# Optimization experiments

Hardware: AMD Instinct MI355X
Metric: run time of the kernel (lower is better)

The kernel has to match this reference:

```python
import jax, jax.numpy as jnp
import numpy as np

NUM_HEADS = 12
KSIZE = 3
PAD = 1


def setup_inputs() -> dict:
    key = jax.random.key(0)
    ks = jax.random.split(key, 5)
    B, H, W, C = 4, 96, 96, 192
    x = jax.random.normal(ks[0], (B, H * W, C), jnp.float32)
    Wq = jax.random.normal(ks[1], (W, W), jnp.float32) * 0.02
    bq = jnp.zeros((W,), jnp.float32)
    Wkv = jax.random.normal(ks[2], (2 * W, W), jnp.float32) * 0.02
    bkv = jnp.zeros((2 * W,), jnp.float32)
    Wp = jax.random.normal(ks[3], (C, C), jnp.float32) * 0.02
    bp = jnp.zeros((C,), jnp.float32)
    f_qr = jnp.float32(1.0)
    f_kr = jnp.float32(1.0)
    f_vr = jnp.float32(1.0)
    return {"x": x, "Wq": Wq, "bq": bq, "Wkv": Wkv, "bkv": bkv, "Wp": Wp,
            "bp": bp, "f_qr": f_qr, "f_kr": f_kr, "f_vr": f_vr, "H": H, "W": W}


def reference(x, Wq, bq, Wkv, bkv, Wp, bp, f_qr, f_kr, f_vr, H, W):
    B, N, C = x.shape
    nh = NUM_HEADS
    hc = C // nh
    scale = C ** (-0.5)
    # faithful to torch: raw reshape of (B, N, C) into (B, C, H, W)
    xn = x.reshape(B, C, H, W)
    # q_proj is Linear over the last (width) axis, size Hw == W
    q = jnp.einsum('bchw,vw->bchv', xn, Wq) + bq            # (B,C,H,W)
    q = q.reshape(B, H, W, nh, hc).transpose(0, 3, 1, 2, 4)  # (B,nh,H,W,hc)
    q = (q * scale * f_qr).reshape(B, nh, H * W, hc)         # (B,nh,L,hc)
    # kv_proj: Linear(W -> 2W) over last axis
    kv = jnp.einsum('bchw,vw->bchv', xn, Wkv) + bkv          # (B,C,H,2W)
    kv = kv.reshape(B, H, W, 2, nh, hc).transpose(3, 0, 4, 5, 1, 2)  # (2,B,nh,hc,H,W)
    kv = jnp.pad(kv, ((0, 0),) * 4 + ((PAD, PAD), (PAD, PAD)))       # zero-pad spatial
    # unfold: 3x3 sliding windows, stride 1 -> one window per pixel
    patches = jnp.stack([kv[..., i:i + H, j:j + W]
                         for i in range(KSIZE) for j in range(KSIZE)], axis=4)
    # (2,B,nh,hc,9,H,W) -> (2,B,nh,L,9,hc); kernel index = kh*3+kw matches nn.Unfold
    patches = patches.reshape(2, B, nh, hc, KSIZE * KSIZE, H * W).transpose(0, 1, 2, 5, 4, 3)
    k = patches[0] * f_kr                                    # (B,nh,L,9,hc)
    v = patches[1] * f_vr
    attn = jax.nn.softmax(jnp.einsum('bnlc,bnlkc->bnlk', q, k), axis=-1)  # (B,nh,L,9)
    out = jnp.einsum('bnlk,bnlkc->bnlc', attn, v)            # (B,nh,L,hc)
    out = out.transpose(0, 2, 1, 3).reshape(B, H, W, C)      # (B,H,W,C)
    out = jnp.einsum('bhwc,oc->bhwo', out, Wp) + bp          # proj Linear(dim,dim)
    return out.reshape(B, H * W, C)
```

## Files before the change

### kernel.cpp

```cpp
#include <hip/hip_runtime.h>

#define HW2   96
#define NH    12
#define LPIX  (HW2*HW2)
#define BATCH 4

typedef __attribute__((ext_vector_type(8))) short bf16x8;
typedef __attribute__((ext_vector_type(4))) float f32x4;

static __device__ __forceinline__ float bf2f(unsigned short u) {
  union { unsigned int i; float f; } v; v.i = ((unsigned int)u) << 16; return v.f;
}
static __device__ __forceinline__ unsigned short f2bf(float f) {
  union { float f; unsigned int i; } v; v.f = f;
  unsigned int r = v.i + 0x7FFF + ((v.i >> 16) & 1);
  return (unsigned short)(r >> 16);
}

__global__ __launch_bounds__(256) void cvt_w_kernel(
    const float* __restrict__ Wq, const float* __restrict__ Wkv,
    const float* __restrict__ Wp,
    unsigned short* __restrict__ wqb, unsigned short* __restrict__ wkvb,
    unsigned short* __restrict__ wpb) {
  int i = blockIdx.x * 256 + threadIdx.x;
  if (i < 9216)       wqb[i]          = f2bf(Wq[i]);
  else if (i < 27648) wkvb[i - 9216]  = f2bf(Wkv[i - 9216]);
  else if (i < 64512) wpb[i - 27648]  = f2bf(Wp[i - 27648]);
}

__global__ __launch_bounds__(256, 4) void qkv_gemm(
    const float* __restrict__ X,
    const unsigned short* __restrict__ wq, const unsigned short* __restrict__ wkv,
    const float* __restrict__ bq, const float* __restrict__ bkv,
    const float* __restrict__ fqr, const float* __restrict__ fkr,
    const float* __restrict__ fvr,
    unsigned short* __restrict__ Qb, unsigned short* __restrict__ KVb)
{
  const int tid  = threadIdx.x;
  const int r0   = blockIdx.x * 64;
  const int lane = tid & 63, w = tid >> 6;
  const int col  = lane & 15;
  const int koff = (lane >> 4) * 8;
  const int arow = r0 + 16 * w + (lane & 15);
  const int rbase = r0 + 16 * w + 4 * (lane >> 4);

  const float* xr = X + (size_t)arow * 96;
  float xv[24];
  *(float4*)&xv[0]  = *(const float4*)(xr + koff);
  *(float4*)&xv[4]  = *(const float4*)(xr + koff + 4);
  *(float4*)&xv[8]  = *(const float4*)(xr + koff + 32);
  *(float4*)&xv[12] = *(const float4*)(xr + koff + 36);
  *(float4*)&xv[16] = *(const float4*)(xr + koff + 64);
  *(float4*)&xv[20] = *(const float4*)(xr + koff + 68);
  unsigned short au[24];
  #pragma unroll
  for (int j = 0; j < 24; j++) au[j] = f2bf(xv[j]);
  bf16x8 af0 = *(const bf16x8*)&au[0];
  bf16x8 af1 = *(const bf16x8*)&au[8];
  bf16x8 af2 = *(const bf16x8*)&au[16];

  const float fqr0 = fqr[0] * 0.07216878364870322f;
  const float fkr0 = fkr[0], fvr0 = fvr[0];

  #pragma unroll
  for (int g = 0; g < 6; g++) {
    bf16x8 bw0[3], bw1[3], bw2[3];
    #pragma unroll
    for (int j = 0; j < 3; j++) {
      int nt = g * 3 + j;
      const unsigned short* wrow = (nt < 6)
          ? wq  + (size_t)(nt * 16 + col) * 96 + koff
          : wkv + (size_t)((nt - 6) * 16 + col) * 96 + koff;
      bw0[j] = *(const bf16x8*)(wrow);
      bw1[j] = *(const bf16x8*)(wrow + 32);
      bw2[j] = *(const bf16x8*)(wrow + 64);
    }
    asm volatile("" ::: "memory");

    #pragma unroll
    for (int j = 0; j < 3; j++) {
      int nt = g * 3 + j;
      f32x4 acc = {0.f, 0.f, 0.f, 0.f};
      acc = __builtin_amdgcn_mfma_f32_16x16x32_bf16(af0, bw0[j], acc, 0, 0, 0);
      acc = __builtin_amdgcn_mfma_f32_16x16x32_bf16(af1, bw1[j], acc, 0, 0, 0);
      acc = __builtin_amdgcn_mfma_f32_16x16x32_bf16(af2, bw2[j], acc, 0, 0, 0);

      if (nt < 6) {
        int u = nt * 16 + col;
        float bias = bq[u];
        #pragma unroll
        for (int i = 0; i < 4; i++)
          Qb[(size_t)(rbase + i) * 96 + u] = f2bf((acc[i] + bias) * fqr0);
      } else {
        int u = (nt - 6) * 16 + col;
        float bias = bkv[u];
        #pragma unroll
        for (int i = 0; i < 4; i++) {
          float s = (i & 1) ? fvr0 : fkr0;
          KVb[(size_t)(rbase + i) * 192 + u] = f2bf((acc[i] + bias) * s);
        }
      }
    }
  }
}

__global__ __launch_bounds__(384, 1) void attnproj_kernel(
    const unsigned short* __restrict__ Qb, const unsigned short* __restrict__ KVb,
    const unsigned short* __restrict__ wp, const float* __restrict__ bp,
    float* __restrict__ Out)
{
  __shared__ unsigned short s_out[32 * 204];
  const int tid = threadIdx.x;
  const int bid = (blockIdx.x & 7) * 144 + (blockIdx.x >> 3);
  const int bl0 = bid * 32;

  {
    const int n  = tid % NH;
    const int pl = tid / NH;
    const int bl = bl0 + pl;
    const int l  = bl % LPIX;
    const int b  = bl / LPIX;
    const int h2 = l / HW2, w2 = l - h2 * HW2;

    const unsigned short* qp = Qb + (size_t)bl * 192 + n * 16;
    uint4 qA = *(const uint4*)(qp);
    uint4 qB = *(const uint4*)(qp + 8);

    const unsigned short* kvb = KVb + (size_t)b * (LPIX * 384) + n * 16;

    int  nbo[9];
    bool okk[9];
    uint4 kA[9], kB[9], vA[9], vB[9];
    #pragma unroll
    for (int kk = 0; kk < 9; kk++) {
      int hh = h2 + kk / 3 - 1;
      int ww = w2 + kk % 3 - 1;
      okk[kk] = ((unsigned)hh < (unsigned)HW2) && ((unsigned)ww < (unsigned)HW2);
      int hc = min(max(hh, 0), HW2 - 1);
      int wc = min(max(ww, 0), HW2 - 1);
      nbo[kk] = (hc * HW2 + wc) * 384;
      const unsigned short* kp = kvb + nbo[kk];
      kA[kk] = *(const uint4*)(kp);
      kB[kk] = *(const uint4*)(kp + 8);
    }
    #pragma unroll
    for (int kk = 0; kk < 9; kk++) {
      const unsigned short* vp = kvb + nbo[kk] + 192;
      vA[kk] = *(const uint4*)(vp);
      vB[kk] = *(const uint4*)(vp + 8);
    }
    asm volatile("" ::: "memory");

    float q[16];
    {
      const unsigned short* qs = (const unsigned short*)&qA;
      #pragma unroll
      for (int j = 0; j < 8; j++) q[j] = bf2f(qs[j]);
      qs = (const unsigned short*)&qB;
      #pragma unroll
      for (int j = 0; j < 8; j++) q[8 + j] = bf2f(qs[j]);
    }

    float sc[9];
    #pragma unroll
    for (int kk = 0; kk < 9; kk++) {
      float s = 0.f;
      const unsigned short* kd = (const unsigned short*)&kA[kk];
      #pragma unroll
      for (int j = 0; j < 8; j++) s = fmaf(q[j], bf2f(kd[j]), s);
      kd = (const unsigned short*)&kB[kk];
      #pragma unroll
      for (int j = 0; j < 8; j++) s = fmaf(q[8 + j], bf2f(kd[j]), s);
      sc[kk] = okk[kk] ? s : 0.f;
    }

    float m = sc[0];
    #pragma unroll
    for (int kk = 1; kk < 9; kk++) m = fmaxf(m, sc[kk]);
    float ssum = 0.f;
    #pragma unroll
    for (int kk = 0; kk < 9; kk++) {
      float e = __expf(sc[kk] - m);
      sc[kk] = e;
      ssum += e;
    }

    float acc[16];
    #pragma unroll
    for (int j = 0; j < 16; j++) acc[j] = 0.f;
    #pragma unroll
    for (int kk = 0; kk < 9; kk++) {
      float wgt = okk[kk] ? sc[kk] : 0.f;
      const unsigned short* vd = (const unsigned short*)&vA[kk];
      #pragma unroll
      for (int j = 0; j < 8; j++) acc[j] = fmaf(wgt, bf2f(vd[j]), acc[j]);
      vd = (const unsigned short*)&vB[kk];
      #pragma unroll
      for (int j = 0; j < 8; j++) acc[8 + j] = fmaf(wgt, bf2f(vd[j]), acc[8 + j]);
    }
    float rinv = 1.f / ssum;
    unsigned short od[16];
    #pragma unroll
    for (int j = 0; j < 16; j++) od[j] = f2bf(acc[j] * rinv);
    unsigned short* op = s_out + pl * 204 + n * 16;
    *(uint4*)(op)     = *(uint4*)&od[0];
    *(uint4*)(op + 8) = *(uint4*)&od[8];
  }
  __syncthreads();

  const int lane = tid & 63, w = tid >> 6;
  const int wr = w & 1, wh = w >> 1;
  const int col  = lane & 15;
  const int koff = (lane >> 4) * 8;
  const int arow = 16 * wr + (lane & 15);
  const int rbase = bl0 + 16 * wr + 4 * (lane >> 4);

  bf16x8 af[6];
  #pragma unroll
  for (int kt = 0; kt < 6; kt++)
    af[kt] = *(const bf16x8*)&s_out[arow * 204 + koff + kt * 32];

  bf16x8 bw[4][6];
  #pragma unroll
  for (int t4 = 0; t4 < 4; t4++) {
    int nt = wh * 4 + t4;
    const unsigned short* wrow = wp + (size_t)(nt * 16 + col) * 192 + koff;
    #pragma unroll
    for (int kt = 0; kt < 6; kt++)
      bw[t4][kt] = *(const bf16x8*)(wrow + kt * 32);
  }
  asm volatile("" ::: "memory");

  #pragma unroll
  for (int t4 = 0; t4 < 4; t4++) {
    int nt = wh * 4 + t4;
    f32x4 acc = {0.f, 0.f, 0.f, 0.f};
    #pragma unroll
    for (int kt = 0; kt < 6; kt++)
      acc = __builtin_amdgcn_mfma_f32_16x16x32_bf16(af[kt], bw[t4][kt], acc, 0, 0, 0);
    int u = nt * 16 + col;
    float bias = bp[u];
    #pragma unroll
    for (int i = 0; i < 4; i++)
      Out[(size_t)(rbase + i) * 192 + u] = acc[i] + bias;
  }
}

extern "C" void kernel_launch(void* const* d_in, const int* in_sizes, int n_in,
                              void* d_out, int out_size, void* d_ws, size_t ws_size,
                              hipStream_t stream) {
  const float* x   = (const float*)d_in[0];
  const float* Wq  = (const float*)d_in[1];
  const float* bq  = (const float*)d_in[2];
  const float* Wkv = (const float*)d_in[3];
  const float* bkv = (const float*)d_in[4];
  const float* Wp  = (const float*)d_in[5];
  const float* bp  = (const float*)d_in[6];
  const float* fqr = (const float*)d_in[7];
  const float* fkr = (const float*)d_in[8];
  const float* fvr = (const float*)d_in[9];

  char* ws = (char*)d_ws;
  unsigned short* Qb   = (unsigned short*)ws;
  unsigned short* KVb  = (unsigned short*)(ws + 14155776);
  unsigned short* wqb  = (unsigned short*)(ws + 42467328);
  unsigned short* wkvb = (unsigned short*)(ws + 42485760);
  unsigned short* wpb  = (unsigned short*)(ws + 42522624);

  cvt_w_kernel<<<dim3(252), dim3(256), 0, stream>>>(Wq, Wkv, Wp, wqb, wkvb, wpb);

  qkv_gemm<<<dim3(1152), dim3(256), 0, stream>>>(
      x, wqb, wkvb, bq, bkv, fqr, fkr, fvr, Qb, KVb);

  attnproj_kernel<<<dim3(1152), dim3(384), 0, stream>>>(
      Qb, KVb, wpb, bp, (float*)d_out);
}
```

Before: 74.61 us.

## Double rows per block in QKV GEMM and attention-projection kernels

Both kernels now process twice as many rows per block (128 rows in the QKV GEMM, 64 pixels in the attention/projection kernel), with the grid halved. Each loaded weight fragment is reused across two row tiles, and in the attention kernel the V loads are issued after the score computation to stagger register pressure. The aim is to amortise weight loads and per-block overhead and raise memory-level parallelism per thread. The cost is higher register use (launch-bounds occupancy hints were removed), fewer blocks to spread across CUs, and larger shared memory per block.

```diff
diff --git a/kernel.cpp b/kernel.cpp
--- a/kernel.cpp
+++ b/kernel.cpp
@@ -28,7 +28,7 @@
   else if (i < 64512) wpb[i - 27648]  = f2bf(Wp[i - 27648]);
 }
 
-__global__ __launch_bounds__(256, 4) void qkv_gemm(
+__global__ __launch_bounds__(256) void qkv_gemm(
     const float* __restrict__ X,
     const unsigned short* __restrict__ wq, const unsigned short* __restrict__ wkv,
     const float* __restrict__ bq, const float* __restrict__ bkv,
@@ -37,27 +37,31 @@
     unsigned short* __restrict__ Qb, unsigned short* __restrict__ KVb)
 {
   const int tid  = threadIdx.x;
-  const int r0   = blockIdx.x * 64;
+  const int r0   = blockIdx.x * 128;
   const int lane = tid & 63, w = tid >> 6;
   const int col  = lane & 15;
   const int koff = (lane >> 4) * 8;
-  const int arow = r0 + 16 * w + (lane & 15);
-  const int rbase = r0 + 16 * w + 4 * (lane >> 4);
-
-  const float* xr = X + (size_t)arow * 96;
-  float xv[24];
-  *(float4*)&xv[0]  = *(const float4*)(xr + koff);
-  *(float4*)&xv[4]  = *(const float4*)(xr + koff + 4);
-  *(float4*)&xv[8]  = *(const float4*)(xr + koff + 32);
-  *(float4*)&xv[12] = *(const float4*)(xr + koff + 36);
-  *(float4*)&xv[16] = *(const float4*)(xr + koff + 64);
-  *(float4*)&xv[20] = *(const float4*)(xr + koff + 68);
-  unsigned short au[24];
+  const int arow0 = r0 + 16 * w + (lane & 15);
+  const int rb0   = r0 + 16 * w + 4 * (lane >> 4);
+
+  bf16x8 af[2][3];
   #pragma unroll
-  for (int j = 0; j < 24; j++) au[j] = f2bf(xv[j]);
-  bf16x8 af0 = *(const bf16x8*)&au[0];
-  bf16x8 af1 = *(const bf16x8*)&au[8];
-  bf16x8 af2 = *(const bf16x8*)&au[16];
+  for (int t = 0; t < 2; t++) {
+    const float* xr = X + (size_t)(arow0 + 64 * t) * 96;
+    float xv[24];
+    *(float4*)&xv[0]  = *(const float4*)(xr + koff);
+    *(float4*)&xv[4]  = *(const float4*)(xr + koff + 4);
+    *(float4*)&xv[8]  = *(const float4*)(xr + koff + 32);
+    *(float4*)&xv[12] = *(const float4*)(xr + koff + 36);
+    *(float4*)&xv[16] = *(const float4*)(xr + koff + 64);
+    *(float4*)&xv[20] = *(const float4*)(xr + koff + 68);
+    unsigned short au[24];
+    #pragma unroll
+    for (int j = 0; j < 24; j++) au[j] = f2bf(xv[j]);
+    af[t][0] = *(const bf16x8*)&au[0];
+    af[t][1] = *(const bf16x8*)&au[8];
+    af[t][2] = *(const bf16x8*)&au[16];
+  }
 
   const float fqr0 = fqr[0] * 0.07216878364870322f;
   const float fkr0 = fkr[0], fvr0 = fvr[0];
@@ -80,131 +84,149 @@
     #pragma unroll
     for (int j = 0; j < 3; j++) {
       int nt = g * 3 + j;
-      f32x4 acc = {0.f, 0.f, 0.f, 0.f};
-      acc = __builtin_amdgcn_mfma_f32_16x16x32_bf16(af0, bw0[j], acc, 0, 0, 0);
-      acc = __builtin_amdgcn_mfma_f32_16x16x32_bf16(af1, bw1[j], acc, 0, 0, 0);
-      acc = __builtin_amdgcn_mfma_f32_16x16x32_bf16(af2, bw2[j], acc, 0, 0, 0);
+      f32x4 acc[2];
+      #pragma unroll
+      for (int t = 0; t < 2; t++) {
+        f32x4 a = {0.f, 0.f, 0.f, 0.f};
+        a = __builtin_amdgcn_mfma_f32_16x16x32_bf16(af[t][0], bw0[j], a, 0, 0, 0);
+        a = __builtin_amdgcn_mfma_f32_16x16x32_bf16(af[t][1], bw1[j], a, 0, 0, 0);
+        a = __builtin_amdgcn_mfma_f32_16x16x32_bf16(af[t][2], bw2[j], a, 0, 0, 0);
+        acc[t] = a;
+      }
 
       if (nt < 6) {
         int u = nt * 16 + col;
         float bias = bq[u];
         #pragma unroll
-        for (int i = 0; i < 4; i++)
-          Qb[(size_t)(rbase + i) * 96 + u] = f2bf((acc[i] + bias) * fqr0);
+        for (int t = 0; t < 2; t++)
+          #pragma unroll
+          for (int i = 0; i < 4; i++)
+            Qb[(size_t)(rb0 + 64 * t + i) * 96 + u] = f2bf((acc[t][i] + bias) * fqr0);
       } else {
         int u = (nt - 6) * 16 + col;
         float bias = bkv[u];
         #pragma unroll
-        for (int i = 0; i < 4; i++) {
-          float s = (i & 1) ? fvr0 : fkr0;
-          KVb[(size_t)(rbase + i) * 192 + u] = f2bf((acc[i] + bias) * s);
-        }
-      }
-    }
-  }
-}
-
-__global__ __launch_bounds__(384, 1) void attnproj_kernel(
+        for (int t = 0; t < 2; t++)
+          #pragma unroll
+          for (int i = 0; i < 4; i++) {
+            float s = (i & 1) ? fvr0 : fkr0;
+            KVb[(size_t)(rb0 + 64 * t + i) * 192 + u] = f2bf((acc[t][i] + bias) * s);
+          }
+      }
+    }
+  }
+}
+
+__global__ __launch_bounds__(384) void attnproj_kernel(
     const unsigned short* __restrict__ Qb, const unsigned short* __restrict__ KVb,
     const unsigned short* __restrict__ wp, const float* __restrict__ bp,
     float* __restrict__ Out)
 {
-  __shared__ unsigned short s_out[32 * 204];
+  __shared__ unsigned short s_out[64 * 204];
   const int tid = threadIdx.x;
-  const int bid = (blockIdx.x & 7) * 144 + (blockIdx.x >> 3);
-  const int bl0 = bid * 32;
+  const int bid = (blockIdx.x & 7) * 72 + (blockIdx.x >> 3);
+  const int bl0 = bid * 64;
 
   {
-    const int n  = tid % NH;
-    const int pl = tid / NH;
-    const int bl = bl0 + pl;
-    const int l  = bl % LPIX;
-    const int b  = bl / LPIX;
-    const int h2 = l / HW2, w2 = l - h2 * HW2;
-
-    const unsigned short* qp = Qb + (size_t)bl * 192 + n * 16;
-    uint4 qA = *(const uint4*)(qp);
-    uint4 qB = *(const uint4*)(qp + 8);
-
+    const int n   = tid % NH;
+    const int pl0 = tid / NH;
+    const int b   = bl0 / LPIX;
     const unsigned short* kvb = KVb + (size_t)b * (LPIX * 384) + n * 16;
 
-    int  nbo[9];
-    bool okk[9];
-    uint4 kA[9], kB[9], vA[9], vB[9];
-    #pragma unroll
-    for (int kk = 0; kk < 9; kk++) {
-      int hh = h2 + kk / 3 - 1;
-      int ww = w2 + kk % 3 - 1;
-      okk[kk] = ((unsigned)hh < (unsigned)HW2) && ((unsigned)ww < (unsigned)HW2);
-      int hc = min(max(hh, 0), HW2 - 1);
-      int wc = min(max(ww, 0), HW2 - 1);
-      nbo[kk] = (hc * HW2 + wc) * 384;
-      const unsigned short* kp = kvb + nbo[kk];
-      kA[kk] = *(const uint4*)(kp);
-      kB[kk] = *(const uint4*)(kp + 8);
-    }
-    #pragma unroll
-    for (int kk = 0; kk < 9; kk++) {
-      const unsigned short* vp = kvb + nbo[kk] + 192;
-      vA[kk] = *(const uint4*)(vp);
-      vB[kk] = *(const uint4*)(vp + 8);
+    int  nbo[2][9];
+    bool okk[2][9];
+    uint4 qA[2], qB[2], kA[2][9], kB[2][9];
+
+    #pragma unroll
+    for (int t = 0; t < 2; t++) {
+      int pl = pl0 + 32 * t;
+      int l  = (bl0 + pl) % LPIX;
+      int h2 = l / HW2, w2 = l - h2 * HW2;
+      #pragma unroll
+      for (int kk = 0; kk < 9; kk++) {
+        int hh = h2 + kk / 3 - 1;
+        int ww = w2 + kk % 3 - 1;
+        okk[t][kk] = ((unsigned)hh < (unsigned)HW2) && ((unsigned)ww < (unsigned)HW2);
+        int hc = min(max(hh, 0), HW2 - 1);
+        int wc = min(max(ww, 0), HW2 - 1);
+        nbo[t][kk] = (hc * HW2 + wc) * 384;
+        const unsigned short* kp = kvb + nbo[t][kk];
+        kA[t][kk] = *(const uint4*)(kp);
+        kB[t][kk] = *(const uint4*)(kp + 8);
+      }
+      const unsigned short* qp = Qb + (size_t)(bl0 + pl) * 192 + n * 16;
+      qA[t] = *(const uint4*)(qp);
+      qB[t] = *(const uint4*)(qp + 8);
     }
     asm volatile("" ::: "memory");
 
-    float q[16];
-    {
-      const unsigned short* qs = (const unsigned short*)&qA;
+    float sc[2][9];
+    #pragma unroll
+    for (int t = 0; t < 2; t++) {
+      float q[16];
+      const unsigned short* qs = (const unsigned short*)&qA[t];
       #pragma unroll
       for (int j = 0; j < 8; j++) q[j] = bf2f(qs[j]);
-      qs = (const unsigned short*)&qB;
+      qs = (const unsigned short*)&qB[t];
       #pragma unroll
       for (int j = 0; j < 8; j++) q[8 + j] = bf2f(qs[j]);
-    }
-
-    float sc[9];
-    #pragma unroll
-    for (int kk = 0; kk < 9; kk++) {
-      float s = 0.f;
-      const unsigned short* kd = (const unsigned short*)&kA[kk];
-      #pragma unroll
-      for (int j = 0; j < 8; j++) s = fmaf(q[j], bf2f(kd[j]), s);
-      kd = (const unsigned short*)&kB[kk];
-      #pragma unroll
-      for (int j = 0; j < 8; j++) s = fmaf(q[8 + j], bf2f(kd[j]), s);
-      sc[kk] = okk[kk] ? s : 0.f;
-    }
-
-    float m = sc[0];
-    #pragma unroll
-    for (int kk = 1; kk < 9; kk++) m = fmaxf(m, sc[kk]);
-    float ssum = 0.f;
-    #pragma unroll
-    for (int kk = 0; kk < 9; kk++) {
-      float e = __expf(sc[kk] - m);
-      sc[kk] = e;
-      ssum += e;
-    }
-
-    float acc[16];
-    #pragma unroll
-    for (int j = 0; j < 16; j++) acc[j] = 0.f;
-    #pragma unroll
-    for (int kk = 0; kk < 9; kk++) {
-      float wgt = okk[kk] ? sc[kk] : 0.f;
-      const unsigned short* vd = (const unsigned short*)&vA[kk];
-      #pragma unroll
-      for (int j = 0; j < 8; j++) acc[j] = fmaf(wgt, bf2f(vd[j]), acc[j]);
-      vd = (const unsigned short*)&vB[kk];
-      #pragma unroll
-      for (int j = 0; j < 8; j++) acc[8 + j] = fmaf(wgt, bf2f(vd[j]), acc[8 + j]);
-    }
-    float rinv = 1.f / ssum;
-    unsigned short od[16];
-    #pragma unroll
-    for (int j = 0; j < 16; j++) od[j] = f2bf(acc[j] * rinv);
-    unsigned short* op = s_out + pl * 204 + n * 16;
-    *(uint4*)(op)     = *(uint4*)&od[0];
-    *(uint4*)(op + 8) = *(uint4*)&od[8];
+      #pragma unroll
+      for (int kk = 0; kk < 9; kk++) {
+        float s = 0.f;
+        const unsigned short* kd = (const unsigned short*)&kA[t][kk];
+        #pragma unroll
+        for (int j = 0; j < 8; j++) s = fmaf(q[j], bf2f(kd[j]), s);
+        kd = (const unsigned short*)&kB[t][kk];
+        #pragma unroll
+        for (int j = 0; j < 8; j++) s = fmaf(q[8 + j], bf2f(kd[j]), s);
+        sc[t][kk] = okk[t][kk] ? s : 0.f;
+      }
+    }
+
+    uint4 vA[2][9], vB[2][9];
+    #pragma unroll
+    for (int t = 0; t < 2; t++)
+      #pragma unroll
+      for (int kk = 0; kk < 9; kk++) {
+        const unsigned short* vp = kvb + nbo[t][kk] + 192;
+        vA[t][kk] = *(const uint4*)(vp);
+        vB[t][kk] = *(const uint4*)(vp + 8);
+      }
+    asm volatile("" ::: "memory");
+
+    #pragma unroll
+    for (int t = 0; t < 2; t++) {
+      float m = sc[t][0];
+      #pragma unroll
+      for (int kk = 1; kk < 9; kk++) m = fmaxf(m, sc[t][kk]);
+      float ssum = 0.f;
+      #pragma unroll
+      for (int kk = 0; kk < 9; kk++) {
+        float e = __expf(sc[t][kk] - m);
+        sc[t][kk] = e;
+        ssum += e;
+      }
+      float acc[16];
+      #pragma unroll
+      for (int j = 0; j < 16; j++) acc[j] = 0.f;
+      #pragma unroll
+      for (int kk = 0; kk < 9; kk++) {
+        float wgt = okk[t][kk] ? sc[t][kk] : 0.f;
+        const unsigned short* vd = (const unsigned short*)&vA[t][kk];
+        #pragma unroll
+        for (int j = 0; j < 8; j++) acc[j] = fmaf(wgt, bf2f(vd[j]), acc[j]);
+        vd = (const unsigned short*)&vB[t][kk];
+        #pragma unroll
+        for (int j = 0; j < 8; j++) acc[8 + j] = fmaf(wgt, bf2f(vd[j]), acc[8 + j]);
+      }
+      float rinv = 1.f / ssum;
+      unsigned short od[16];
+      #pragma unroll
+      for (int j = 0; j < 16; j++) od[j] = f2bf(acc[j] * rinv);
+      unsigned short* op = s_out + (pl0 + 32 * t) * 204 + n * 16;
+      *(uint4*)(op)     = *(uint4*)&od[0];
+      *(uint4*)(op + 8) = *(uint4*)&od[8];
+    }
   }
   __syncthreads();
 
@@ -212,37 +234,38 @@
   const int wr = w & 1, wh = w >> 1;
   const int col  = lane & 15;
   const int koff = (lane >> 4) * 8;
-  const int arow = 16 * wr + (lane & 15);
-  const int rbase = bl0 + 16 * wr + 4 * (lane >> 4);
-
-  bf16x8 af[6];
+
+  bf16x8 af[2][6];
   #pragma unroll
-  for (int kt = 0; kt < 6; kt++)
-    af[kt] = *(const bf16x8*)&s_out[arow * 204 + koff + kt * 32];
-
-  bf16x8 bw[4][6];
+  for (int rg = 0; rg < 2; rg++) {
+    int arow = 32 * wr + 16 * rg + (lane & 15);
+    #pragma unroll
+    for (int kt = 0; kt < 6; kt++)
+      af[rg][kt] = *(const bf16x8*)&s_out[arow * 204 + koff + kt * 32];
+  }
+
   #pragma unroll
   for (int t4 = 0; t4 < 4; t4++) {
     int nt = wh * 4 + t4;
     const unsigned short* wrow = wp + (size_t)(nt * 16 + col) * 192 + koff;
-    #pragma unroll
-    for (int kt = 0; kt < 6; kt++)
-      bw[t4][kt] = *(const bf16x8*)(wrow + kt * 32);
-  }
-  asm volatile("" ::: "memory");
-
-  #pragma unroll
-  for (int t4 = 0; t4 < 4; t4++) {
-    int nt = wh * 4 + t4;
-    f32x4 acc = {0.f, 0.f, 0.f, 0.f};
-    #pragma unroll
-    for (int kt = 0; kt < 6; kt++)
-      acc = __builtin_amdgcn_mfma_f32_16x16x32_bf16(af[kt], bw[t4][kt], acc, 0, 0, 0);
+    bf16x8 bw[6];
+    #pragma unroll
+    for (int kt = 0; kt < 6; kt++) bw[kt] = *(const bf16x8*)(wrow + kt * 32);
+    asm volatile("" ::: "memory");
+
     int u = nt * 16 + col;
     float bias = bp[u];
     #pragma unroll
-    for (int i = 0; i < 4; i++)
-      Out[(size_t)(rbase + i) * 192 + u] = acc[i] + bias;
+    for (int rg = 0; rg < 2; rg++) {
+      f32x4 acc = {0.f, 0.f, 0.f, 0.f};
+      #pragma unroll
+      for (int kt = 0; kt < 6; kt++)
+        acc = __builtin_amdgcn_mfma_f32_16x16x32_bf16(af[rg][kt], bw[kt], acc, 0, 0, 0);
+      int rbase = bl0 + 32 * wr + 16 * rg + 4 * (lane >> 4);
+      #pragma unroll
+      for (int i = 0; i < 4; i++)
+        Out[(size_t)(rbase + i) * 192 + u] = acc[i] + bias;
+    }
   }
 }
 
@@ -269,9 +292,9 @@
 
   cvt_w_kernel<<<dim3(252), dim3(256), 0, stream>>>(Wq, Wkv, Wp, wqb, wkvb, wpb);
 
-  qkv_gemm<<<dim3(1152), dim3(256), 0, stream>>>(
+  qkv_gemm<<<dim3(576), dim3(256), 0, stream>>>(
       x, wqb, wkvb, bq, bkv, fqr, fkr, fvr, Qb, KVb);
 
-  attnproj_kernel<<<dim3(1152), dim3(384), 0, stream>>>(
+  attnproj_kernel<<<dim3(576), dim3(384), 0, stream>>>(
       Qb, KVb, wpb, bp, (float*)d_out);
 }
```

Result: faster. 66.20 us (-11.3%).
